# Performance work log

Hardware: AMD Instinct MI355X
Metric: run time of the kernel (lower is better)

Reference implementation:

```python
import jax, jax.numpy as jnp
import numpy as np

B, S, D, H = 16384, 3, 512, 8
HD = D // H
FF = 4 * D
EPS = 1e-5


def _layernorm(x, g, b):
    mu = jnp.mean(x, axis=-1, keepdims=True)
    var = jnp.mean(jnp.square(x - mu), axis=-1, keepdims=True)
    return (x - mu) * jax.lax.rsqrt(var + EPS) * g + b


def setup_inputs() -> dict:
    key = jax.random.key(0)
    ks = jax.random.split(key, 12)
    s = 0.02
    return {
        "feat0": jax.random.normal(ks[0], (B, D), jnp.float32),
        "feat1": jax.random.normal(ks[1], (B, D), jnp.float32),
        "feat2": jax.random.normal(ks[2], (B, D), jnp.float32),
        "pos_emb": jax.random.normal(ks[3], (S, D), jnp.float32) * s,
        "w_in": jax.random.normal(ks[4], (3 * D, D), jnp.float32) * s,  # packed q,k,v proj (torch layout)
        "b_in": jnp.zeros((3 * D,), jnp.float32),
        "w_out": jax.random.normal(ks[5], (D, D), jnp.float32) * s,
        "b_out": jnp.zeros((D,), jnp.float32),
        "ln1_g": jnp.ones((D,), jnp.float32),
        "ln1_b": jnp.zeros((D,), jnp.float32),
        "w1": jax.random.normal(ks[6], (FF, D), jnp.float32) * s,
        "b1": jnp.zeros((FF,), jnp.float32),
        "w2": jax.random.normal(ks[7], (D, FF), jnp.float32) * s,
        "b2": jnp.zeros((D,), jnp.float32),
        "ln2_g": jnp.ones((D,), jnp.float32),
        "ln2_b": jnp.zeros((D,), jnp.float32),
    }


def reference(feat0, feat1, feat2, pos_emb, w_in, b_in, w_out, b_out,
              ln1_g, ln1_b, w1, b1, w2, b2, ln2_g, ln2_b):
    # stack modalities -> [B, S=3, D]; add position embedding
    x = jnp.stack([feat0, feat1, feat2], axis=1) + pos_emb

    # self-attention (torch MHA math: packed in-proj, per-head scaled dot product)
    qkv = jnp.einsum("bsd,ed->bse", x, w_in) + b_in  # [B,S,3D]
    q, k, v = jnp.split(qkv, 3, axis=-1)
    q = q.reshape(B, S, H, HD)
    k = k.reshape(B, S, H, HD)
    v = v.reshape(B, S, H, HD)
    scores = jnp.einsum("bqhd,bkhd->bhqk", q, k) / jnp.sqrt(jnp.float32(HD))
    attn = jax.nn.softmax(scores, axis=-1)  # [B,H,S,S] (need_weights path)
    o = jnp.einsum("bhqk,bkhd->bqhd", attn, v).reshape(B, S, D)
    o = jnp.einsum("bsd,ed->bse", o, w_out) + b_out

    # residual + norm1 (dropout is identity in eval)
    x = _layernorm(x + o, ln1_g, ln1_b)

    # feed-forward: relu MLP
    h = jax.nn.relu(jnp.einsum("bsd,fd->bsf", x, w1) + b1)
    ff = jnp.einsum("bsf,df->bsd", h, w2) + b2
    x = _layernorm(x + ff, ln2_g, ln2_b)

    # adaptive avg pool over seq dim -> [B, D]
    return jnp.mean(x, axis=1)
```

## Files before the change

kernel.cpp:

```cpp
#include <hip/hip_runtime.h>
#include <hip/hip_bf16.h>


#define BTOT 16384
#define DD 512
#define EPS_ 1e-5f

typedef __attribute__((ext_vector_type(8))) short bf8v;
typedef __attribute__((ext_vector_type(4))) float f4v;

__device__ __forceinline__ unsigned short f2bf(float f) {
  unsigned int u = __builtin_bit_cast(unsigned int, f);
  u += 0x7fffu + ((u >> 16) & 1u);
  return (unsigned short)(u >> 16);
}
__device__ __forceinline__ float bf2f(unsigned short s) {
  unsigned int u = ((unsigned int)s) << 16;
  return __builtin_bit_cast(float, u);
}
__device__ __forceinline__ unsigned int pk2(float a, float b) {
  return (unsigned int)f2bf(a) | ((unsigned int)f2bf(b) << 16);
}

#define GLDS16(gp, lp)                                                   \
  __builtin_amdgcn_global_load_lds(                                      \
      (const __attribute__((address_space(1))) void*)(gp),               \
      (__attribute__((address_space(3))) void*)(lp), 16, 0, 0)

__global__ __launch_bounds__(256) void cast_w(const float* __restrict__ w,
                                              unsigned short* __restrict__ o, int n) {
  int i = (blockIdx.x * 256 + threadIdx.x) * 4;
  if (i >= n) return;
  float4 v = *(const float4*)&w[i];
  uint2 u; u.x = pk2(v.x, v.y); u.y = pk2(v.z, v.w);
  *(uint2*)&o[i] = u;
}

__global__ __launch_bounds__(256) void build_x(const float* __restrict__ f0,
                                               const float* __restrict__ f1,
                                               const float* __restrict__ f2,
                                               const float* __restrict__ pos,
                                               unsigned short* __restrict__ xbf, int b0) {
  int gi = blockIdx.x * 256 + threadIdx.x;
  int e = gi * 4;
  int r = e >> 9;
  int d = e & 511;
  int bl = r / 3, s = r - bl * 3;
  const float* f = (s == 0 ? f0 : (s == 1 ? f1 : f2)) + (size_t)(b0 + bl) * DD + d;
  const float* pp = pos + s * DD + d;
  float4 fv = *(const float4*)f;
  float4 pv = *(const float4*)pp;
  uint2 o; o.x = pk2(fv.x + pv.x, fv.y + pv.y); o.y = pk2(fv.z + pv.z, fv.w + pv.w);
  *(uint2*)&xbf[(size_t)r * DD + d] = o;
}

#define TM 128
#define TN 128
#define BKK 64

template <int ACT, int OBF>
__global__ __launch_bounds__(256, 2) void gemm_bt(const unsigned short* __restrict__ A,
                                                  const unsigned short* __restrict__ Bw,
                                                  const float* __restrict__ bias,
                                                  void* __restrict__ C, int M, int N, int K) {
  __shared__ unsigned short lA[TM * BKK];
  __shared__ unsigned short lB[TN * BKK];
  const int tid = threadIdx.x;
  const int row0 = blockIdx.y * TM;
  const int col0 = blockIdx.x * TN;
  const int lane = tid & 63;
  const int wid = tid >> 6;
  const int wm = (wid >> 1) * 64;
  const int wn = (wid & 1) * 64;
  const int lr = lane & 15;
  const int ql = lane >> 4;
  const int xk = lr & 7;

  f4v acc[4][4];
#pragma unroll
  for (int i = 0; i < 4; i++)
#pragma unroll
    for (int j = 0; j < 4; j++) acc[i][j] = (f4v)0.f;

  const int c0 = wid * 4;
  const int srow = lane >> 3;
  const int sq = (lane & 7) ^ srow;
  const unsigned short* Ag0 = A + (size_t)(row0 + c0 * 8 + srow) * K + sq * 8;
  const unsigned short* Bg0 = Bw + (size_t)(col0 + c0 * 8 + srow) * K + sq * 8;
  unsigned short* lA0 = &lA[c0 * 512];
  unsigned short* lB0 = &lB[c0 * 512];

  for (int k0 = 0; k0 < K; k0 += BKK) {
#pragma unroll
    for (int i = 0; i < 4; i++) {
      GLDS16(Ag0 + (size_t)(i * 8) * K + k0, lA0 + i * 512);
      GLDS16(Bg0 + (size_t)(i * 8) * K + k0, lB0 + i * 512);
    }
    __syncthreads();
#pragma unroll
    for (int kk = 0; kk < BKK; kk += 32) {
      const int slot = (((kk >> 3) + ql) ^ xk) * 8;
      bf8v af[4], bfr[4];
#pragma unroll
      for (int i = 0; i < 4; i++)
        af[i] = *(const bf8v*)&lA[(wm + i * 16 + lr) * BKK + slot];
#pragma unroll
      for (int j = 0; j < 4; j++)
        bfr[j] = *(const bf8v*)&lB[(wn + j * 16 + lr) * BKK + slot];
#pragma unroll
      for (int i = 0; i < 4; i++)
#pragma unroll
        for (int j = 0; j < 4; j++)
          acc[i][j] = __builtin_amdgcn_mfma_f32_16x16x32_bf16(af[i], bfr[j], acc[i][j], 0, 0, 0);
    }
    __syncthreads();
  }

#pragma unroll
  for (int j = 0; j < 4; j++) {
    int gcol = col0 + wn + j * 16 + lr;
    float bv = bias[gcol];
#pragma unroll
    for (int i = 0; i < 4; i++) {
#pragma unroll
      for (int r = 0; r < 4; r++) {
        int grow = row0 + wm + i * 16 + (lane >> 4) * 4 + r;
        float v = acc[i][j][r] + bv;
        if (ACT) v = fmaxf(v, 0.f);
        if (OBF)
          ((unsigned short*)C)[(size_t)grow * N + gcol] = f2bf(v);
        else
          ((float*)C)[(size_t)grow * N + gcol] = v;
      }
    }
  }
}

__global__ __launch_bounds__(512) void attn_k(const unsigned short* __restrict__ qkv,
                                              unsigned short* __restrict__ ob) {
  int b = blockIdx.x;
  int h = threadIdx.x >> 6;
  int lane = threadIdx.x & 63;
  size_t base = ((size_t)b * 3) * 1536 + h * 64 + lane;
  float q[3], k[3], v[3];
#pragma unroll
  for (int s = 0; s < 3; s++) {
    q[s] = bf2f(qkv[base + (size_t)s * 1536]);
    k[s] = bf2f(qkv[base + (size_t)s * 1536 + 512]);
    v[s] = bf2f(qkv[base + (size_t)s * 1536 + 1024]);
  }
  float sc[3][3];
#pragma unroll
  for (int qi = 0; qi < 3; qi++)
#pragma unroll
    for (int ki = 0; ki < 3; ki++) {
      float p = q[qi] * k[ki];
#pragma unroll
      for (int off = 32; off > 0; off >>= 1) p += __shfl_xor(p, off, 64);
      sc[qi][ki] = p * 0.125f;
    }
#pragma unroll
  for (int qi = 0; qi < 3; qi++) {
    float m = fmaxf(sc[qi][0], fmaxf(sc[qi][1], sc[qi][2]));
    float e0 = __expf(sc[qi][0] - m), e1 = __expf(sc[qi][1] - m), e2 = __expf(sc[qi][2] - m);
    float inv = 1.f / (e0 + e1 + e2);
    float o = (e0 * v[0] + e1 * v[1] + e2 * v[2]) * inv;
    ob[((size_t)b * 3 + qi) * DD + h * 64 + lane] = f2bf(o);
  }
}

__global__ __launch_bounds__(256) void ln1_k(const float* __restrict__ y,
                                             const float* __restrict__ f0,
                                             const float* __restrict__ f1,
                                             const float* __restrict__ f2,
                                             const float* __restrict__ pos,
                                             const float* __restrict__ g,
                                             const float* __restrict__ be,
                                             unsigned short* __restrict__ x1, int b0) {
  int wid = threadIdx.x >> 6, lane = threadIdx.x & 63;
  int r = blockIdx.x * 4 + wid;
  int bl = r / 3, s = r - bl * 3;
  const float* f = (s == 0 ? f0 : (s == 1 ? f1 : f2)) + (size_t)(b0 + bl) * DD;
  const float* pp = pos + s * DD;
  const float* yy = y + (size_t)r * DD;
  int d = lane * 8;
  float x[8];
#pragma unroll
  for (int i = 0; i < 8; i++) x[i] = f[d + i] + pp[d + i] + yy[d + i];
  float su = 0.f, sq = 0.f;
#pragma unroll
  for (int i = 0; i < 8; i++) { su += x[i]; sq += x[i] * x[i]; }
#pragma unroll
  for (int off = 32; off > 0; off >>= 1) {
    su += __shfl_xor(su, off, 64);
    sq += __shfl_xor(sq, off, 64);
  }
  float mean = su * (1.f / 512.f);
  float var = sq * (1.f / 512.f) - mean * mean;
  float rs = rsqrtf(var + EPS_);
  unsigned short o[8];
#pragma unroll
  for (int i = 0; i < 8; i++) o[i] = f2bf((x[i] - mean) * rs * g[d + i] + be[d + i]);
  uint4 pack;
  pack.x = (unsigned)o[0] | ((unsigned)o[1] << 16);
  pack.y = (unsigned)o[2] | ((unsigned)o[3] << 16);
  pack.z = (unsigned)o[4] | ((unsigned)o[5] << 16);
  pack.w = (unsigned)o[6] | ((unsigned)o[7] << 16);
  *(uint4*)&x1[(size_t)r * DD + d] = pack;
}

__global__ __launch_bounds__(192) void final_k(const unsigned short* __restrict__ x1,
                                               const float* __restrict__ ff,
                                               const float* __restrict__ g,
                                               const float* __restrict__ be,
                                               float* __restrict__ out) {
  __shared__ float t3[3][DD];
  int w = threadIdx.x >> 6, lane = threadIdx.x & 63;
  int b = blockIdx.x;
  size_t r = (size_t)b * 3 + w;
  int d = lane * 8;
  float x[8];
#pragma unroll
  for (int i = 0; i < 8; i++) x[i] = bf2f(x1[r * DD + d + i]) + ff[r * DD + d + i];
  float su = 0.f, sq = 0.f;
#pragma unroll
  for (int i = 0; i < 8; i++) { su += x[i]; sq += x[i] * x[i]; }
#pragma unroll
  for (int off = 32; off > 0; off >>= 1) {
    su += __shfl_xor(su, off, 64);
    sq += __shfl_xor(sq, off, 64);
  }
  float mean = su * (1.f / 512.f);
  float var = sq * (1.f / 512.f) - mean * mean;
  float rs = rsqrtf(var + EPS_);
#pragma unroll
  for (int i = 0; i < 8; i++) t3[w][d + i] = (x[i] - mean) * rs * g[d + i] + be[d + i];
  __syncthreads();
  for (int dd = threadIdx.x; dd < DD; dd += 192)
    out[(size_t)b * DD + dd] = (t3[0][dd] + t3[1][dd] + t3[2][dd]) * (1.f / 3.f);
}

extern "C" void kernel_launch(void* const* d_in, const int* in_sizes, int n_in,
                              void* d_out, int out_size, void* d_ws, size_t ws_size,
                              hipStream_t stream) {
  const float* feat0 = (const float*)d_in[0];
  const float* feat1 = (const float*)d_in[1];
  const float* feat2 = (const float*)d_in[2];
  const float* pos   = (const float*)d_in[3];
  const float* w_in  = (const float*)d_in[4];
  const float* b_in  = (const float*)d_in[5];
  const float* w_out = (const float*)d_in[6];
  const float* b_out = (const float*)d_in[7];
  const float* ln1_g = (const float*)d_in[8];
  const float* ln1_b = (const float*)d_in[9];
  const float* w1    = (const float*)d_in[10];
  const float* b1    = (const float*)d_in[11];
  const float* w2    = (const float*)d_in[12];
  const float* b2    = (const float*)d_in[13];
  const float* ln2_g = (const float*)d_in[14];
  const float* ln2_b = (const float*)d_in[15];
  float* out = (float*)d_out;

  char* p = (char*)d_ws;
  unsigned short* w_in_b  = (unsigned short*)p; p += (size_t)1536 * 512 * 2;
  unsigned short* w_out_b = (unsigned short*)p; p += (size_t)512 * 512 * 2;
  unsigned short* w1_b    = (unsigned short*)p; p += (size_t)2048 * 512 * 2;
  unsigned short* w2_b    = (unsigned short*)p; p += (size_t)512 * 2048 * 2;
  size_t wbytes = (size_t)(p - (char*)d_ws);

  int nch = 16;
  for (int c = 1; c <= 16; c <<= 1) {
    size_t rows = (size_t)(BTOT / c) * 3;
    if (wbytes + rows * 9216 <= ws_size) { nch = c; break; }
  }
  const int Bc = BTOT / nch;
  const int rows = Bc * 3;

  unsigned short* xbf = (unsigned short*)p;
  char* regB = p + (size_t)rows * 1024;
  unsigned short* ob = (unsigned short*)(regB + (size_t)rows * 3072);
  unsigned short* hb = ob + (size_t)rows * 512;

  cast_w<<<768, 256, 0, stream>>>(w_in, w_in_b, 1536 * 512);
  cast_w<<<256, 256, 0, stream>>>(w_out, w_out_b, 512 * 512);
  cast_w<<<1024, 256, 0, stream>>>(w1, w1_b, 2048 * 512);
  cast_w<<<1024, 256, 0, stream>>>(w2, w2_b, 512 * 2048);

  for (int c = 0; c < nch; c++) {
    int b0 = c * Bc;
    build_x<<<rows / 2, 256, 0, stream>>>(feat0, feat1, feat2, pos, xbf, b0);
    gemm_bt<0, 1><<<dim3(12, rows / 128), 256, 0, stream>>>(
        xbf, w_in_b, b_in, (void*)regB, rows, 1536, 512);
    attn_k<<<Bc, 512, 0, stream>>>((const unsigned short*)regB, ob);
    gemm_bt<0, 0><<<dim3(4, rows / 128), 256, 0, stream>>>(
        ob, w_out_b, b_out, (void*)regB, rows, 512, 512);
    ln1_k<<<rows / 4, 256, 0, stream>>>((const float*)regB, feat0, feat1, feat2, pos,
                                        ln1_g, ln1_b, xbf, b0);
    gemm_bt<1, 1><<<dim3(16, rows / 128), 256, 0, stream>>>(
        xbf, w1_b, b1, (void*)hb, rows, 2048, 512);
    gemm_bt<0, 0><<<dim3(4, rows / 128), 256, 0, stream>>>(
        hb, w2_b, b2, (void*)regB, rows, 512, 2048);
    final_k<<<Bc, 192, 0, stream>>>(xbf, (const float*)regB, ln2_g, ln2_b,
                                    out + (size_t)b0 * DD);
  }
}
```

Baseline: 769.8 us.

## Double-buffer GEMM K-loop with async LDS loads and fuse residual into epilogue

Rewrites the bf16 MFMA GEMM main loop to use two 32-wide K stages in LDS with a new swizzle. The next stage is prefetched via global_load_lds while the current one is consumed, using explicit vmcnt waits and barriers instead of load-then-sync. Residual additions are folded into the out-proj and FFN2 GEMM epilogues, so the layernorm kernels read a single fp32 tensor with vector loads. The attention residual now uses the bf16-rounded input instead of fp32 features plus position embedding, which slightly changes precision.

```diff
diff --git a/kernel.cpp b/kernel.cpp
--- a/kernel.cpp
+++ b/kernel.cpp
@@ -26,6 +26,10 @@
   __builtin_amdgcn_global_load_lds(                                      \
       (const __attribute__((address_space(1))) void*)(gp),               \
       (__attribute__((address_space(3))) void*)(lp), 16, 0, 0)
+
+#define WAIT_VM4 0x0F74
+#define WAIT_VM0 0x0F70
+#define CFENCE() __asm__ volatile("" ::: "memory")
 
 __global__ __launch_bounds__(256) void cast_w(const float* __restrict__ w,
                                               unsigned short* __restrict__ o, int n) {
@@ -56,25 +60,25 @@
 
 #define TM 128
 #define TN 128
-#define BKK 64
-
-template <int ACT, int OBF>
+
+template <int ACT, int OBF, int RES>
 __global__ __launch_bounds__(256, 2) void gemm_bt(const unsigned short* __restrict__ A,
                                                   const unsigned short* __restrict__ Bw,
                                                   const float* __restrict__ bias,
+                                                  const unsigned short* __restrict__ res,
                                                   void* __restrict__ C, int M, int N, int K) {
-  __shared__ unsigned short lA[TM * BKK];
-  __shared__ unsigned short lB[TN * BKK];
+  __shared__ unsigned short lA[2][TM * 32];
+  __shared__ unsigned short lB[2][TN * 32];
   const int tid = threadIdx.x;
   const int row0 = blockIdx.y * TM;
   const int col0 = blockIdx.x * TN;
   const int lane = tid & 63;
-  const int wid = tid >> 6;
-  const int wm = (wid >> 1) * 64;
-  const int wn = (wid & 1) * 64;
+  const int w = tid >> 6;
+  const int wm = (w >> 1) * 64;
+  const int wn = (w & 1) * 64;
   const int lr = lane & 15;
   const int ql = lane >> 4;
-  const int xk = lr & 7;
+  const int fslot = (ql ^ ((lr >> 1) & 3)) * 8;
 
   f4v acc[4][4];
 #pragma unroll
@@ -82,39 +86,50 @@
 #pragma unroll
     for (int j = 0; j < 4; j++) acc[i][j] = (f4v)0.f;
 
-  const int c0 = wid * 4;
-  const int srow = lane >> 3;
-  const int sq = (lane & 7) ^ srow;
-  const unsigned short* Ag0 = A + (size_t)(row0 + c0 * 8 + srow) * K + sq * 8;
-  const unsigned short* Bg0 = Bw + (size_t)(col0 + c0 * 8 + srow) * K + sq * 8;
-  unsigned short* lA0 = &lA[c0 * 512];
-  unsigned short* lB0 = &lB[c0 * 512];
-
-  for (int k0 = 0; k0 < K; k0 += BKK) {
-#pragma unroll
-    for (int i = 0; i < 4; i++) {
-      GLDS16(Ag0 + (size_t)(i * 8) * K + k0, lA0 + i * 512);
-      GLDS16(Bg0 + (size_t)(i * 8) * K + k0, lB0 + i * 512);
-    }
-    __syncthreads();
-#pragma unroll
-    for (int kk = 0; kk < BKK; kk += 32) {
-      const int slot = (((kk >> 3) + ql) ^ xk) * 8;
-      bf8v af[4], bfr[4];
-#pragma unroll
-      for (int i = 0; i < 4; i++)
-        af[i] = *(const bf8v*)&lA[(wm + i * 16 + lr) * BKK + slot];
+  const int srow = w * 32 + (lane >> 2);
+  const int gq8 = (((lane & 3) ^ ((lane >> 3) & 3)) << 3);
+  const unsigned short* AgB = A + (size_t)(row0 + srow) * K + gq8;
+  const unsigned short* BgB = Bw + (size_t)(col0 + srow) * K + gq8;
+  const int lds0 = (w * 32) * 32;
+  const int lds1 = (w * 32 + 16) * 32;
+
+#define STAGE(buf, kk)                                  \
+  {                                                     \
+    GLDS16(AgB + (kk), &lA[buf][lds0]);                 \
+    GLDS16(AgB + (size_t)16 * K + (kk), &lA[buf][lds1]);\
+    GLDS16(BgB + (kk), &lB[buf][lds0]);                 \
+    GLDS16(BgB + (size_t)16 * K + (kk), &lB[buf][lds1]);\
+  }
+
+  STAGE(0, 0)
+  STAGE(1, 32)
+  int cur = 0;
+
+  for (int k0 = 0; k0 < K; k0 += 32) {
+    CFENCE();
+    if (k0 + 32 < K) __builtin_amdgcn_s_waitcnt(WAIT_VM4);
+    else             __builtin_amdgcn_s_waitcnt(WAIT_VM0);
+    __builtin_amdgcn_s_barrier();
+    CFENCE();
+    bf8v af[4], bfr[4];
+#pragma unroll
+    for (int i = 0; i < 4; i++)
+      af[i] = *(const bf8v*)&lA[cur][(wm + i * 16 + lr) * 32 + fslot];
+#pragma unroll
+    for (int j = 0; j < 4; j++)
+      bfr[j] = *(const bf8v*)&lB[cur][(wn + j * 16 + lr) * 32 + fslot];
+#pragma unroll
+    for (int i = 0; i < 4; i++)
 #pragma unroll
       for (int j = 0; j < 4; j++)
-        bfr[j] = *(const bf8v*)&lB[(wn + j * 16 + lr) * BKK + slot];
-#pragma unroll
-      for (int i = 0; i < 4; i++)
-#pragma unroll
-        for (int j = 0; j < 4; j++)
-          acc[i][j] = __builtin_amdgcn_mfma_f32_16x16x32_bf16(af[i], bfr[j], acc[i][j], 0, 0, 0);
-    }
-    __syncthreads();
-  }
+        acc[i][j] = __builtin_amdgcn_mfma_f32_16x16x32_bf16(af[i], bfr[j], acc[i][j], 0, 0, 0);
+    CFENCE();
+    __builtin_amdgcn_s_barrier();
+    CFENCE();
+    if (k0 + 64 < K) STAGE(cur, k0 + 64)
+    cur ^= 1;
+  }
+#undef STAGE
 
 #pragma unroll
   for (int j = 0; j < 4; j++) {
@@ -126,6 +141,7 @@
       for (int r = 0; r < 4; r++) {
         int grow = row0 + wm + i * 16 + (lane >> 4) * 4 + r;
         float v = acc[i][j][r] + bv;
+        if (RES) v += bf2f(res[(size_t)grow * N + gcol]);
         if (ACT) v = fmaxf(v, 0.f);
         if (OBF)
           ((unsigned short*)C)[(size_t)grow * N + gcol] = f2bf(v);
@@ -169,24 +185,16 @@
   }
 }
 
-__global__ __launch_bounds__(256) void ln1_k(const float* __restrict__ y,
-                                             const float* __restrict__ f0,
-                                             const float* __restrict__ f1,
-                                             const float* __restrict__ f2,
-                                             const float* __restrict__ pos,
-                                             const float* __restrict__ g,
-                                             const float* __restrict__ be,
-                                             unsigned short* __restrict__ x1, int b0) {
+__global__ __launch_bounds__(256) void ln_row(const float* __restrict__ y,
+                                              const float* __restrict__ g,
+                                              const float* __restrict__ be,
+                                              unsigned short* __restrict__ xo) {
   int wid = threadIdx.x >> 6, lane = threadIdx.x & 63;
-  int r = blockIdx.x * 4 + wid;
-  int bl = r / 3, s = r - bl * 3;
-  const float* f = (s == 0 ? f0 : (s == 1 ? f1 : f2)) + (size_t)(b0 + bl) * DD;
-  const float* pp = pos + s * DD;
-  const float* yy = y + (size_t)r * DD;
+  size_t r = (size_t)blockIdx.x * 4 + wid;
   int d = lane * 8;
-  float x[8];
-#pragma unroll
-  for (int i = 0; i < 8; i++) x[i] = f[d + i] + pp[d + i] + yy[d + i];
+  float4 a = *(const float4*)&y[r * DD + d];
+  float4 b = *(const float4*)&y[r * DD + d + 4];
+  float x[8] = {a.x, a.y, a.z, a.w, b.x, b.y, b.z, b.w};
   float su = 0.f, sq = 0.f;
 #pragma unroll
   for (int i = 0; i < 8; i++) { su += x[i]; sq += x[i] * x[i]; }
@@ -206,11 +214,10 @@
   pack.y = (unsigned)o[2] | ((unsigned)o[3] << 16);
   pack.z = (unsigned)o[4] | ((unsigned)o[5] << 16);
   pack.w = (unsigned)o[6] | ((unsigned)o[7] << 16);
-  *(uint4*)&x1[(size_t)r * DD + d] = pack;
-}
-
-__global__ __launch_bounds__(192) void final_k(const unsigned short* __restrict__ x1,
-                                               const float* __restrict__ ff,
+  *(uint4*)&xo[r * DD + d] = pack;
+}
+
+__global__ __launch_bounds__(192) void final_k(const float* __restrict__ ff,
                                                const float* __restrict__ g,
                                                const float* __restrict__ be,
                                                float* __restrict__ out) {
@@ -219,9 +226,9 @@
   int b = blockIdx.x;
   size_t r = (size_t)b * 3 + w;
   int d = lane * 8;
-  float x[8];
-#pragma unroll
-  for (int i = 0; i < 8; i++) x[i] = bf2f(x1[r * DD + d + i]) + ff[r * DD + d + i];
+  float4 a = *(const float4*)&ff[r * DD + d];
+  float4 bb = *(const float4*)&ff[r * DD + d + 4];
+  float x[8] = {a.x, a.y, a.z, a.w, bb.x, bb.y, bb.z, bb.w};
   float su = 0.f, sq = 0.f;
 #pragma unroll
   for (int i = 0; i < 8; i++) { su += x[i]; sq += x[i] * x[i]; }
@@ -289,18 +296,17 @@
   for (int c = 0; c < nch; c++) {
     int b0 = c * Bc;
     build_x<<<rows / 2, 256, 0, stream>>>(feat0, feat1, feat2, pos, xbf, b0);
-    gemm_bt<0, 1><<<dim3(12, rows / 128), 256, 0, stream>>>(
-        xbf, w_in_b, b_in, (void*)regB, rows, 1536, 512);
+    gemm_bt<0, 1, 0><<<dim3(12, rows / 128), 256, 0, stream>>>(
+        xbf, w_in_b, b_in, nullptr, (void*)regB, rows, 1536, 512);
     attn_k<<<Bc, 512, 0, stream>>>((const unsigned short*)regB, ob);
-    gemm_bt<0, 0><<<dim3(4, rows / 128), 256, 0, stream>>>(
-        ob, w_out_b, b_out, (void*)regB, rows, 512, 512);
-    ln1_k<<<rows / 4, 256, 0, stream>>>((const float*)regB, feat0, feat1, feat2, pos,
-                                        ln1_g, ln1_b, xbf, b0);
-    gemm_bt<1, 1><<<dim3(16, rows / 128), 256, 0, stream>>>(
-        xbf, w1_b, b1, (void*)hb, rows, 2048, 512);
-    gemm_bt<0, 0><<<dim3(4, rows / 128), 256, 0, stream>>>(
-        hb, w2_b, b2, (void*)regB, rows, 512, 2048);
-    final_k<<<Bc, 192, 0, stream>>>(xbf, (const float*)regB, ln2_g, ln2_b,
+    gemm_bt<0, 0, 1><<<dim3(4, rows / 128), 256, 0, stream>>>(
+        ob, w_out_b, b_out, xbf, (void*)regB, rows, 512, 512);
+    ln_row<<<rows / 4, 256, 0, stream>>>((const float*)regB, ln1_g, ln1_b, xbf);
+    gemm_bt<1, 1, 0><<<dim3(16, rows / 128), 256, 0, stream>>>(
+        xbf, w1_b, b1, nullptr, (void*)hb, rows, 2048, 512);
+    gemm_bt<0, 0, 1><<<dim3(4, rows / 128), 256, 0, stream>>>(
+        hb, w2_b, b2, xbf, (void*)regB, rows, 512, 2048);
+    final_k<<<Bc, 192, 0, stream>>>((const float*)regB, ln2_g, ln2_b,
                                     out + (size_t)b0 * DD);
   }
 }
```

After: 810.7 us. +5.3%, slower.

## Fuse residuals into GEMM epilogues, write bf16 outputs, and shrink the workspace

Applied to the files above, without the earlier changes.

Residual adds move into the GEMM epilogues. The out-projection now adds the bf16 input x, and the FF2 GEMM adds x1 in place. All intermediates are stored as bf16 instead of fp32, which removes the separate residual loads and cuts global traffic. Attention writes its output in place into the q slot of the qkv buffer. The smaller per-row workspace allows fewer chunks. The four weight casts merge into one launch, and GEMM blocks are remapped so that row tiles are spread across the XCDs. In exchange, the residual stream is held at bf16 precision rather than fp32, which may reduce accuracy.

```diff
diff --git a/kernel.cpp b/kernel.cpp
--- a/kernel.cpp
+++ b/kernel.cpp
@@ -21,19 +21,32 @@
 __device__ __forceinline__ unsigned int pk2(float a, float b) {
   return (unsigned int)f2bf(a) | ((unsigned int)f2bf(b) << 16);
 }
+__device__ __forceinline__ void unpk8(uint4 raw, float* x) {
+  x[0] = bf2f(raw.x & 0xffff); x[1] = bf2f(raw.x >> 16);
+  x[2] = bf2f(raw.y & 0xffff); x[3] = bf2f(raw.y >> 16);
+  x[4] = bf2f(raw.z & 0xffff); x[5] = bf2f(raw.z >> 16);
+  x[6] = bf2f(raw.w & 0xffff); x[7] = bf2f(raw.w >> 16);
+}
 
 #define GLDS16(gp, lp)                                                   \
   __builtin_amdgcn_global_load_lds(                                      \
       (const __attribute__((address_space(1))) void*)(gp),               \
       (__attribute__((address_space(3))) void*)(lp), 16, 0, 0)
 
-__global__ __launch_bounds__(256) void cast_w(const float* __restrict__ w,
-                                              unsigned short* __restrict__ o, int n) {
+__global__ __launch_bounds__(256) void cast_all(const float* __restrict__ wi,
+                                                const float* __restrict__ wo,
+                                                const float* __restrict__ w1,
+                                                const float* __restrict__ w2,
+                                                unsigned short* __restrict__ arena) {
   int i = (blockIdx.x * 256 + threadIdx.x) * 4;
-  if (i >= n) return;
-  float4 v = *(const float4*)&w[i];
+  const float* src; int off;
+  if (i < 786432)       { src = wi; off = 0; }
+  else if (i < 1048576) { src = wo; off = 786432; }
+  else if (i < 2097152) { src = w1; off = 1048576; }
+  else                  { src = w2; off = 2097152; }
+  float4 v = *(const float4*)&src[i - off];
   uint2 u; u.x = pk2(v.x, v.y); u.y = pk2(v.z, v.w);
-  *(uint2*)&o[i] = u;
+  *(uint2*)&arena[i] = u;
 }
 
 __global__ __launch_bounds__(256) void build_x(const float* __restrict__ f0,
@@ -54,24 +67,28 @@
   *(uint2*)&xbf[(size_t)r * DD + d] = o;
 }
 
-#define TM 128
-#define TN 128
-#define BKK 64
-
-template <int ACT, int OBF>
+template <int ACT, int RES>
 __global__ __launch_bounds__(256, 2) void gemm_bt(const unsigned short* __restrict__ A,
+                                                  int lda,
                                                   const unsigned short* __restrict__ Bw,
                                                   const float* __restrict__ bias,
-                                                  void* __restrict__ C, int M, int N, int K) {
-  __shared__ unsigned short lA[TM * BKK];
-  __shared__ unsigned short lB[TN * BKK];
+                                                  const unsigned short* res,
+                                                  unsigned short* C, int ldc,
+                                                  int N, int K) {
+  __shared__ unsigned short lA[128 * 64];
+  __shared__ unsigned short lB[128 * 64];
   const int tid = threadIdx.x;
-  const int row0 = blockIdx.y * TM;
-  const int col0 = blockIdx.x * TN;
+  const int gx = gridDim.x;
+  const int bid = blockIdx.y * gx + blockIdx.x;
+  const int xcd = bid & 7;
+  const int ii = bid >> 3;
+  const int row0 = (xcd + 8 * (ii / gx)) * 128;
+  const int col0 = (ii % gx) * 128;
+
   const int lane = tid & 63;
-  const int wid = tid >> 6;
-  const int wm = (wid >> 1) * 64;
-  const int wn = (wid & 1) * 64;
+  const int w = tid >> 6;
+  const int wm = (w >> 1) * 64;
+  const int wn = (w & 1) * 64;
   const int lr = lane & 15;
   const int ql = lane >> 4;
   const int xk = lr & 7;
@@ -82,31 +99,31 @@
 #pragma unroll
     for (int j = 0; j < 4; j++) acc[i][j] = (f4v)0.f;
 
-  const int c0 = wid * 4;
+  const int c0 = w * 4;
   const int srow = lane >> 3;
   const int sq = (lane & 7) ^ srow;
-  const unsigned short* Ag0 = A + (size_t)(row0 + c0 * 8 + srow) * K + sq * 8;
+  const unsigned short* Ag0 = A + (size_t)(row0 + c0 * 8 + srow) * lda + sq * 8;
   const unsigned short* Bg0 = Bw + (size_t)(col0 + c0 * 8 + srow) * K + sq * 8;
   unsigned short* lA0 = &lA[c0 * 512];
   unsigned short* lB0 = &lB[c0 * 512];
 
-  for (int k0 = 0; k0 < K; k0 += BKK) {
+  for (int k0 = 0; k0 < K; k0 += 64) {
 #pragma unroll
     for (int i = 0; i < 4; i++) {
-      GLDS16(Ag0 + (size_t)(i * 8) * K + k0, lA0 + i * 512);
+      GLDS16(Ag0 + (size_t)(i * 8) * lda + k0, lA0 + i * 512);
       GLDS16(Bg0 + (size_t)(i * 8) * K + k0, lB0 + i * 512);
     }
     __syncthreads();
 #pragma unroll
-    for (int kk = 0; kk < BKK; kk += 32) {
+    for (int kk = 0; kk < 64; kk += 32) {
       const int slot = (((kk >> 3) + ql) ^ xk) * 8;
       bf8v af[4], bfr[4];
 #pragma unroll
       for (int i = 0; i < 4; i++)
-        af[i] = *(const bf8v*)&lA[(wm + i * 16 + lr) * BKK + slot];
+        af[i] = *(const bf8v*)&lA[(wm + i * 16 + lr) * 64 + slot];
 #pragma unroll
       for (int j = 0; j < 4; j++)
-        bfr[j] = *(const bf8v*)&lB[(wn + j * 16 + lr) * BKK + slot];
+        bfr[j] = *(const bf8v*)&lB[(wn + j * 16 + lr) * 64 + slot];
 #pragma unroll
       for (int i = 0; i < 4; i++)
 #pragma unroll
@@ -124,20 +141,17 @@
     for (int i = 0; i < 4; i++) {
 #pragma unroll
       for (int r = 0; r < 4; r++) {
-        int grow = row0 + wm + i * 16 + (lane >> 4) * 4 + r;
+        int grow = row0 + wm + i * 16 + ql * 4 + r;
         float v = acc[i][j][r] + bv;
+        if (RES) v += bf2f(res[(size_t)grow * N + gcol]);
         if (ACT) v = fmaxf(v, 0.f);
-        if (OBF)
-          ((unsigned short*)C)[(size_t)grow * N + gcol] = f2bf(v);
-        else
-          ((float*)C)[(size_t)grow * N + gcol] = v;
+        C[(size_t)grow * ldc + gcol] = f2bf(v);
       }
     }
   }
 }
 
-__global__ __launch_bounds__(512) void attn_k(const unsigned short* __restrict__ qkv,
-                                              unsigned short* __restrict__ ob) {
+__global__ __launch_bounds__(512) void attn_k(unsigned short* __restrict__ qkv) {
   int b = blockIdx.x;
   int h = threadIdx.x >> 6;
   int lane = threadIdx.x & 63;
@@ -165,28 +179,20 @@
     float e0 = __expf(sc[qi][0] - m), e1 = __expf(sc[qi][1] - m), e2 = __expf(sc[qi][2] - m);
     float inv = 1.f / (e0 + e1 + e2);
     float o = (e0 * v[0] + e1 * v[1] + e2 * v[2]) * inv;
-    ob[((size_t)b * 3 + qi) * DD + h * 64 + lane] = f2bf(o);
-  }
-}
-
-__global__ __launch_bounds__(256) void ln1_k(const float* __restrict__ y,
-                                             const float* __restrict__ f0,
-                                             const float* __restrict__ f1,
-                                             const float* __restrict__ f2,
-                                             const float* __restrict__ pos,
-                                             const float* __restrict__ g,
-                                             const float* __restrict__ be,
-                                             unsigned short* __restrict__ x1, int b0) {
+    qkv[base + (size_t)qi * 1536] = f2bf(o);
+  }
+}
+
+__global__ __launch_bounds__(256) void ln_row(const unsigned short* __restrict__ y,
+                                              int ldy,
+                                              const float* __restrict__ g,
+                                              const float* __restrict__ be,
+                                              unsigned short* __restrict__ xo) {
   int wid = threadIdx.x >> 6, lane = threadIdx.x & 63;
-  int r = blockIdx.x * 4 + wid;
-  int bl = r / 3, s = r - bl * 3;
-  const float* f = (s == 0 ? f0 : (s == 1 ? f1 : f2)) + (size_t)(b0 + bl) * DD;
-  const float* pp = pos + s * DD;
-  const float* yy = y + (size_t)r * DD;
+  size_t r = (size_t)blockIdx.x * 4 + wid;
   int d = lane * 8;
   float x[8];
-#pragma unroll
-  for (int i = 0; i < 8; i++) x[i] = f[d + i] + pp[d + i] + yy[d + i];
+  unpk8(*(const uint4*)&y[r * ldy + d], x);
   float su = 0.f, sq = 0.f;
 #pragma unroll
   for (int i = 0; i < 8; i++) { su += x[i]; sq += x[i] * x[i]; }
@@ -206,11 +212,10 @@
   pack.y = (unsigned)o[2] | ((unsigned)o[3] << 16);
   pack.z = (unsigned)o[4] | ((unsigned)o[5] << 16);
   pack.w = (unsigned)o[6] | ((unsigned)o[7] << 16);
-  *(uint4*)&x1[(size_t)r * DD + d] = pack;
-}
-
-__global__ __launch_bounds__(192) void final_k(const unsigned short* __restrict__ x1,
-                                               const float* __restrict__ ff,
+  *(uint4*)&xo[r * DD + d] = pack;
+}
+
+__global__ __launch_bounds__(192) void final_k(const unsigned short* __restrict__ ff,
                                                const float* __restrict__ g,
                                                const float* __restrict__ be,
                                                float* __restrict__ out) {
@@ -220,8 +225,7 @@
   size_t r = (size_t)b * 3 + w;
   int d = lane * 8;
   float x[8];
-#pragma unroll
-  for (int i = 0; i < 8; i++) x[i] = bf2f(x1[r * DD + d + i]) + ff[r * DD + d + i];
+  unpk8(*(const uint4*)&ff[r * DD + d], x);
   float su = 0.f, sq = 0.f;
 #pragma unroll
   for (int i = 0; i < 8; i++) { su += x[i]; sq += x[i] * x[i]; }
@@ -261,46 +265,41 @@
   const float* ln2_b = (const float*)d_in[15];
   float* out = (float*)d_out;
 
-  char* p = (char*)d_ws;
-  unsigned short* w_in_b  = (unsigned short*)p; p += (size_t)1536 * 512 * 2;
-  unsigned short* w_out_b = (unsigned short*)p; p += (size_t)512 * 512 * 2;
-  unsigned short* w1_b    = (unsigned short*)p; p += (size_t)2048 * 512 * 2;
-  unsigned short* w2_b    = (unsigned short*)p; p += (size_t)512 * 2048 * 2;
-  size_t wbytes = (size_t)(p - (char*)d_ws);
+  unsigned short* arena  = (unsigned short*)d_ws;
+  unsigned short* w_in_b  = arena;
+  unsigned short* w_out_b = arena + 786432;
+  unsigned short* w1_b    = arena + 1048576;
+  unsigned short* w2_b    = arena + 2097152;
+  char* p = (char*)d_ws + (size_t)3145728 * 2;
+  const size_t wbytes = (size_t)3145728 * 2;
 
   int nch = 16;
   for (int c = 1; c <= 16; c <<= 1) {
-    size_t rows = (size_t)(BTOT / c) * 3;
-    if (wbytes + rows * 9216 <= ws_size) { nch = c; break; }
+    size_t rws = (size_t)(BTOT / c) * 3;
+    if (wbytes + rws * 5120 <= ws_size) { nch = c; break; }
   }
   const int Bc = BTOT / nch;
   const int rows = Bc * 3;
+  const int RT = rows / 128;
 
   unsigned short* xbf = (unsigned short*)p;
-  char* regB = p + (size_t)rows * 1024;
-  unsigned short* ob = (unsigned short*)(regB + (size_t)rows * 3072);
-  unsigned short* hb = ob + (size_t)rows * 512;
-
-  cast_w<<<768, 256, 0, stream>>>(w_in, w_in_b, 1536 * 512);
-  cast_w<<<256, 256, 0, stream>>>(w_out, w_out_b, 512 * 512);
-  cast_w<<<1024, 256, 0, stream>>>(w1, w1_b, 2048 * 512);
-  cast_w<<<1024, 256, 0, stream>>>(w2, w2_b, 512 * 2048);
+  unsigned short* regB = xbf + (size_t)rows * 512;
+
+  cast_all<<<3072, 256, 0, stream>>>(w_in, w_out, w1, w2, arena);
 
   for (int c = 0; c < nch; c++) {
     int b0 = c * Bc;
     build_x<<<rows / 2, 256, 0, stream>>>(feat0, feat1, feat2, pos, xbf, b0);
-    gemm_bt<0, 1><<<dim3(12, rows / 128), 256, 0, stream>>>(
-        xbf, w_in_b, b_in, (void*)regB, rows, 1536, 512);
-    attn_k<<<Bc, 512, 0, stream>>>((const unsigned short*)regB, ob);
-    gemm_bt<0, 0><<<dim3(4, rows / 128), 256, 0, stream>>>(
-        ob, w_out_b, b_out, (void*)regB, rows, 512, 512);
-    ln1_k<<<rows / 4, 256, 0, stream>>>((const float*)regB, feat0, feat1, feat2, pos,
-                                        ln1_g, ln1_b, xbf, b0);
-    gemm_bt<1, 1><<<dim3(16, rows / 128), 256, 0, stream>>>(
-        xbf, w1_b, b1, (void*)hb, rows, 2048, 512);
-    gemm_bt<0, 0><<<dim3(4, rows / 128), 256, 0, stream>>>(
-        hb, w2_b, b2, (void*)regB, rows, 512, 2048);
-    final_k<<<Bc, 192, 0, stream>>>(xbf, (const float*)regB, ln2_g, ln2_b,
-                                    out + (size_t)b0 * DD);
-  }
-}
+    gemm_bt<0, 0><<<dim3(12, RT), 256, 0, stream>>>(
+        xbf, 512, w_in_b, b_in, nullptr, regB, 1536, 1536, 512);
+    attn_k<<<Bc, 512, 0, stream>>>(regB);
+    gemm_bt<0, 1><<<dim3(4, RT), 256, 0, stream>>>(
+        regB, 1536, w_out_b, b_out, xbf, regB + 512, 1536, 512, 512);
+    ln_row<<<rows / 4, 256, 0, stream>>>(regB + 512, 1536, ln1_g, ln1_b, xbf);
+    gemm_bt<1, 0><<<dim3(16, RT), 256, 0, stream>>>(
+        xbf, 512, w1_b, b1, nullptr, regB, 2048, 2048, 512);
+    gemm_bt<0, 1><<<dim3(4, RT), 256, 0, stream>>>(
+        regB, 2048, w2_b, b2, xbf, xbf, 512, 512, 2048);
+    final_k<<<Bc, 192, 0, stream>>>(xbf, ln2_g, ln2_b, out + (size_t)b0 * DD);
+  }
+}
```

After: 664.0 us. 13.7% less time.
